# Kernel optimization log

Hardware: AMD Instinct MI355X
Metric: run time of the kernel (lower is better)

The kernel has to match this reference:

```python
import jax, jax.numpy as jnp
import numpy as np

NUM_GROUPS = 8
EPS = 1e-6


def group_norm(x, gamma, beta):
    # x: [B, C, N] flattened spatial; GroupNorm over (channels-in-group, spatial)
    B, C, N = x.shape
    xg = x.reshape(B, NUM_GROUPS, C // NUM_GROUPS, N)
    mean = xg.mean(axis=(2, 3), keepdims=True)
    var = xg.var(axis=(2, 3), keepdims=True)
    xn = ((xg - mean) * jax.lax.rsqrt(var + EPS)).reshape(B, C, N)
    return xn * gamma[None, :, None] + beta[None, :, None]


def setup_inputs() -> dict:
    key = jax.random.key(0)
    ks = jax.random.split(key, 3)
    B, C, H, W, D = 4, 128, 16, 16, 16
    x = jax.random.normal(ks[0], (B, C, H, W, D), dtype=jnp.float32)
    gamma = jnp.ones((C,), dtype=jnp.float32)
    beta = jnp.zeros((C,), dtype=jnp.float32)
    init_scale = 0.1
    # default_init(scale): variance-scaling ~ scale/fan_avg uniform; approximate with scaled normal
    w_qkv = jax.random.normal(ks[1], (3 * C, C), dtype=jnp.float32) * np.sqrt(init_scale / C)
    b_qkv = jnp.zeros((3 * C,), dtype=jnp.float32)
    w_proj = jax.random.normal(ks[2], (C, C), dtype=jnp.float32) * np.sqrt(init_scale / C)
    b_proj = jnp.zeros((C,), dtype=jnp.float32)
    return {"x": x, "gamma": gamma, "beta": beta, "w_qkv": w_qkv,
            "b_qkv": b_qkv, "w_proj": w_proj, "b_proj": b_proj}


def reference(x, gamma, beta, w_qkv, b_qkv, w_proj, b_proj):
    B, C, H, W, D = x.shape
    N = H * W * D
    xf = x.reshape(B, C, N)
    xn = group_norm(xf, gamma, beta)
    # 1x1 Conv3d == channel GEMM: [3C, C] @ [B, C, N]
    qkv = jnp.einsum('oc,bcn->bon', w_qkv, xn) + b_qkv[None, :, None]
    q, k, v = jnp.split(qkv, 3, axis=1)  # each [B, C, N]
    scale = float(C) ** (-0.5)
    w = jnp.einsum('bcq,bck->bqk', q, k) * scale  # [B, N, N]
    w = jax.nn.softmax(w, axis=-1)
    h = jnp.einsum('bqk,bck->bcq', w, v)  # [B, C, N]
    h = jnp.einsum('oc,bcn->bon', w_proj, h) + b_proj[None, :, None]
    out = xf + h  # skip_scale = 1.0 (skip_scale=False)
    return out.reshape(B, C, H, W, D)
```

## Files before the change

### kernel.cpp

```cpp
#include <hip/hip_runtime.h>

typedef __bf16 bf16_t;
typedef bf16_t bf16x8 __attribute__((ext_vector_type(8)));
typedef float f32x4 __attribute__((ext_vector_type(4)));
typedef unsigned short u16;
typedef unsigned int u32;

__device__ __forceinline__ float bfu2f(u32 h) {
  union { u32 u; float f; } v; v.u = h << 16;
  return v.f;
}
__device__ __forceinline__ void gll16(const void* g, void* l) {
  __builtin_amdgcn_global_load_lds((const __attribute__((address_space(1))) unsigned int*)g,
                                   (__attribute__((address_space(3))) unsigned int*)l, 16, 0, 0);
}

__global__ __launch_bounds__(256) void gn_stats(const float* __restrict__ x,
                                                float* __restrict__ partial) {
  int bg = blockIdx.x >> 4, ck = blockIdx.x & 15;
  int tid = threadIdx.x;
  const float4* base = reinterpret_cast<const float4*>(x + (size_t)bg * 65536 + ck * 4096);
  float s = 0.f, sq = 0.f;
  #pragma unroll
  for (int j = 0; j < 4; ++j) {
    float4 v = base[j * 256 + tid];
    s += v.x + v.y + v.z + v.w;
    sq += v.x * v.x + v.y * v.y + v.z * v.z + v.w * v.w;
  }
  #pragma unroll
  for (int off = 32; off > 0; off >>= 1) {
    s += __shfl_down(s, off);
    sq += __shfl_down(sq, off);
  }
  __shared__ float red[8];
  int wid = tid >> 6;
  if ((tid & 63) == 0) { red[wid] = s; red[4 + wid] = sq; }
  __syncthreads();
  if (tid == 0) {
    float ts = red[0] + red[1] + red[2] + red[3];
    float tq = red[4] + red[5] + red[6] + red[7];
    partial[(bg * 16 + ck) * 2] = ts;
    partial[(bg * 16 + ck) * 2 + 1] = tq;
  }
}

__global__ __launch_bounds__(256) void gn_norm(const float* __restrict__ x,
                                               const float* __restrict__ gamma,
                                               const float* __restrict__ beta,
                                               const float* __restrict__ partial,
                                               u16* __restrict__ xnt) {
  int bg = blockIdx.x >> 4, ck = blockIdx.x & 15;
  int b = bg >> 3, g = bg & 7;
  int tid = threadIdx.x;
  float s = 0.f, sq = 0.f;
  #pragma unroll
  for (int k = 0; k < 16; ++k) {
    s += partial[(bg * 16 + k) * 2];
    sq += partial[(bg * 16 + k) * 2 + 1];
  }
  float mean = s * (1.f / 65536.f);
  float var = sq * (1.f / 65536.f) - mean * mean;
  float rstd = rsqrtf(var + 1e-6f);
  int c_l = tid & 15;
  int c = g * 16 + c_l;
  float ga = gamma[c] * rstd;
  float be = beta[c] - mean * ga;
  const float* xr = x + ((size_t)(b * 128 + c)) * 4096;
  bf16_t* outb = (bf16_t*)(xnt + (size_t)b * 4096 * 128 + c);
  int n0 = ck * 256 + (tid >> 4);
  #pragma unroll
  for (int i = 0; i < 16; ++i) {
    int n = n0 + i * 16;
    outb[(size_t)n * 128] = (bf16_t)(xr[n] * ga + be);
  }
}

__global__ __launch_bounds__(256) void qkv_kernel(const float* __restrict__ wq,
                                                  const float* __restrict__ bq,
                                                  const u16* __restrict__ xnt,
                                                  u16* __restrict__ qt,
                                                  u16* __restrict__ kt,
                                                  u16* __restrict__ vv) {
  __shared__ char aS[16384];
  __shared__ char bS[16384];
  int b = blockIdx.z;
  int o0 = blockIdx.y * 64;
  int n0 = blockIdx.x * 64;
  int tid = threadIdx.x;
  #pragma unroll
  for (int i = 0; i < 8; ++i) {
    int chunk = tid + (i << 8);
    int o = chunk >> 5, cj = (chunk & 31) << 2;
    float4 f = *reinterpret_cast<const float4*>(wq + (o0 + o) * 128 + cj);
    u16 h0 = __builtin_bit_cast(u16, (bf16_t)f.x);
    u16 h1 = __builtin_bit_cast(u16, (bf16_t)f.y);
    u16 h2 = __builtin_bit_cast(u16, (bf16_t)f.z);
    u16 h3 = __builtin_bit_cast(u16, (bf16_t)f.w);
    ushort4 h4 = make_ushort4(h0, h1, h2, h3);
    *reinterpret_cast<ushort4*>(aS + ((o * 256 + cj * 2) ^ ((o & 7) << 4))) = h4;
  }
  #pragma unroll
  for (int i = 0; i < 4; ++i) {
    int chunk = tid + (i << 8);
    int n = chunk >> 4, ch = chunk & 15;
    uint4 d = *reinterpret_cast<const uint4*>(xnt + ((size_t)(b * 4096 + n0 + n)) * 128 + ch * 8);
    *reinterpret_cast<uint4*>(bS + ((n * 256 + ch * 16) ^ ((n & 7) << 4))) = d;
  }
  __syncthreads();
  int w = tid >> 6, l = tid & 63, lr = l & 15, lg = l >> 4;
  f32x4 acc[4] = {{0,0,0,0},{0,0,0,0},{0,0,0,0},{0,0,0,0}};
  int orow = 16 * w + lr;
  #pragma unroll
  for (int kc = 0; kc < 4; ++kc) {
    int c2 = (lg * 8 + 32 * kc) * 2;
    bf16x8 a = *reinterpret_cast<const bf16x8*>(aS + ((orow * 256 + c2) ^ ((orow & 7) << 4)));
    #pragma unroll
    for (int fn = 0; fn < 4; ++fn) {
      int n = lr + 16 * fn;
      bf16x8 bb = *reinterpret_cast<const bf16x8*>(bS + ((n * 256 + c2) ^ ((n & 7) << 4)));
      acc[fn] = __builtin_amdgcn_mfma_f32_16x16x32_bf16(a, bb, acc[fn], 0, 0, 0);
    }
  }
  const float alpha = 0.12753325f;
  #pragma unroll
  for (int fn = 0; fn < 4; ++fn) {
    #pragma unroll
    for (int j = 0; j < 4; ++j) {
      int o = o0 + 16 * w + lg * 4 + j;
      int n = n0 + lr + 16 * fn;
      float v = acc[fn][j] + bq[o];
      if (o < 128)      ((bf16_t*)qt)[((size_t)(b * 4096 + n)) * 128 + o] = (bf16_t)(v * alpha);
      else if (o < 256) ((bf16_t*)kt)[((size_t)(b * 4096 + n)) * 128 + (o - 128)] = (bf16_t)v;
      else              ((bf16_t*)vv)[((size_t)(b * 128 + (o - 256))) * 4096 + n] = (bf16_t)v;
    }
  }
}

__global__ __launch_bounds__(256) void attn_kernel(const u16* __restrict__ qt,
                                                   const u16* __restrict__ kt,
                                                   const u16* __restrict__ vv,
                                                   u16* __restrict__ opart,
                                                   float* __restrict__ ml) {
  __shared__ char kS[2][16384];
  __shared__ char vS[2][16384];
  __shared__ char pS[8192];
  int b = blockIdx.z;
  int sp = blockIdx.y;
  int q0 = blockIdx.x * 64;
  int tid = threadIdx.x;
  int w = tid >> 6, l = tid & 63, lr = l & 15, lg = l >> 4;

  bf16x8 qa[4];
  {
    const u16* qrow = qt + ((size_t)(b * 4096 + q0 + 16 * w + lr)) * 128 + lg * 8;
    #pragma unroll
    for (int kc = 0; kc < 4; ++kc)
      qa[kc] = *reinterpret_cast<const bf16x8*>(qrow + 32 * kc);
  }
  f32x4 acc[8];
  #pragma unroll
  for (int i = 0; i < 8; ++i) acc[i] = (f32x4){0.f, 0.f, 0.f, 0.f};
  float m2[4], lsum[4];
  #pragma unroll
  for (int j = 0; j < 4; ++j) { m2[j] = -1e30f; lsum[j] = 0.f; }

  const u16* ktb = kt + ((size_t)(b * 4096 + sp * 1024)) * 128;
  const u16* vvb = vv + ((size_t)b * 128) * 4096 + sp * 1024;

  auto stage = [&](int bufi, int kti) {
    #pragma unroll
    for (int i = 0; i < 4; ++i) {
      int n = (tid >> 4) + i * 16;
      int ck = (tid & 15) ^ (n & 7);
      gll16(ktb + (size_t)(kti * 64 + n) * 128 + ck * 8, kS[bufi] + tid * 16 + i * 4096);
    }
    #pragma unroll
    for (int i = 0; i < 4; ++i) {
      int c = (tid >> 3) + i * 32;
      int ck = (tid & 7) ^ (c & 7);
      gll16(vvb + (size_t)c * 4096 + kti * 64 + ck * 8, vS[bufi] + tid * 16 + i * 4096);
    }
  };

  stage(0, 0);
  __syncthreads();
  int buf = 0;

  for (int kti = 0; kti < 16; ++kti) {
    if (kti < 15) stage(buf ^ 1, kti + 1);

    f32x4 s[4];
    #pragma unroll
    for (int fn = 0; fn < 4; ++fn) s[fn] = (f32x4){0.f, 0.f, 0.f, 0.f};
    __builtin_amdgcn_s_setprio(1);
    #pragma unroll
    for (int kc = 0; kc < 4; ++kc) {
      int c2 = (lg * 8 + 32 * kc) * 2;
      bf16x8 a = qa[kc];
      #pragma unroll
      for (int fn = 0; fn < 4; ++fn) {
        int kp = lr + 16 * fn;
        bf16x8 bb = *reinterpret_cast<const bf16x8*>(kS[buf] + ((kp * 256 + c2) ^ ((kp & 7) << 4)));
        s[fn] = __builtin_amdgcn_mfma_f32_16x16x32_bf16(a, bb, s[fn], 0, 0, 0);
      }
    }
    __builtin_amdgcn_s_setprio(0);

    float mt[4];
    #pragma unroll
    for (int j = 0; j < 4; ++j)
      mt[j] = fmaxf(fmaxf(s[0][j], s[1][j]), fmaxf(s[2][j], s[3][j]));
    bool grow = (mt[0] > m2[0] + 8.f) || (mt[1] > m2[1] + 8.f) ||
                (mt[2] > m2[2] + 8.f) || (mt[3] > m2[3] + 8.f);
    if (__any(grow)) {
      #pragma unroll
      for (int off = 1; off < 16; off <<= 1)
        #pragma unroll
        for (int j = 0; j < 4; ++j)
          mt[j] = fmaxf(mt[j], __shfl_xor(mt[j], off));
      float r[4];
      #pragma unroll
      for (int j = 0; j < 4; ++j) {
        float mn = fmaxf(m2[j], mt[j]);
        r[j] = exp2f(m2[j] - mn);
        m2[j] = mn;
        lsum[j] *= r[j];
      }
      #pragma unroll
      for (int fc = 0; fc < 8; ++fc)
        #pragma unroll
        for (int j = 0; j < 4; ++j) acc[fc][j] *= r[j];
    }
    #pragma unroll
    for (int fn = 0; fn < 4; ++fn)
      #pragma unroll
      for (int j = 0; j < 4; ++j) {
        float p = exp2f(s[fn][j] - m2[j]);
        lsum[j] += p;
        int qg = 16 * w + lg * 4 + j;
        int kp = lr + 16 * fn;
        *reinterpret_cast<bf16_t*>(pS + ((qg * 128 + kp * 2) ^ ((qg & 7) << 4))) = (bf16_t)p;
      }
    __builtin_amdgcn_s_setprio(1);
    #pragma unroll
    for (int kc = 0; kc < 2; ++kc) {
      int qg = 16 * w + lr;
      int k2 = (lg * 8 + 32 * kc) * 2;
      bf16x8 pa = *reinterpret_cast<const bf16x8*>(pS + ((qg * 128 + k2) ^ ((qg & 7) << 4)));
      #pragma unroll
      for (int fc = 0; fc < 8; ++fc) {
        int c = lr + 16 * fc;
        bf16x8 vb = *reinterpret_cast<const bf16x8*>(vS[buf] + ((c * 128 + k2) ^ ((c & 7) << 4)));
        acc[fc] = __builtin_amdgcn_mfma_f32_16x16x32_bf16(pa, vb, acc[fc], 0, 0, 0);
      }
    }
    __builtin_amdgcn_s_setprio(0);
    __syncthreads();
    buf ^= 1;
  }
  #pragma unroll
  for (int off = 1; off < 16; off <<= 1)
    #pragma unroll
    for (int j = 0; j < 4; ++j)
      lsum[j] += __shfl_xor(lsum[j], off);
  #pragma unroll
  for (int j = 0; j < 4; ++j) {
    int nloc = 16 * w + lg * 4 + j;
    size_t row = (size_t)(sp * 16384 + b * 4096 + q0 + nloc);
    bf16_t* orow = (bf16_t*)(opart + row * 128 + lr);
    #pragma unroll
    for (int fc = 0; fc < 8; ++fc)
      orow[16 * fc] = (bf16_t)(acc[fc][j]);
    if (lr == 0) {
      ml[row * 2] = m2[j];
      ml[row * 2 + 1] = lsum[j];
    }
  }
}

__global__ __launch_bounds__(256) void proj_kernel(const float* __restrict__ wp,
                                                   const float* __restrict__ bp,
                                                   const u16* __restrict__ opart,
                                                   const float* __restrict__ ml,
                                                   const float* __restrict__ x,
                                                   float* __restrict__ out) {
  __shared__ char aS[16384];
  __shared__ char bS[16384];
  int b = blockIdx.z;
  int o0 = blockIdx.y * 64;
  int n0 = blockIdx.x * 64;
  int tid = threadIdx.x;
  #pragma unroll
  for (int i = 0; i < 8; ++i) {
    int chunk = tid + (i << 8);
    int o = chunk >> 5, cj = (chunk & 31) << 2;
    float4 f = *reinterpret_cast<const float4*>(wp + (o0 + o) * 128 + cj);
    u16 h0 = __builtin_bit_cast(u16, (bf16_t)f.x);
    u16 h1 = __builtin_bit_cast(u16, (bf16_t)f.y);
    u16 h2 = __builtin_bit_cast(u16, (bf16_t)f.z);
    u16 h3 = __builtin_bit_cast(u16, (bf16_t)f.w);
    *reinterpret_cast<ushort4*>(aS + ((o * 256 + cj * 2) ^ ((o & 7) << 4))) = make_ushort4(h0, h1, h2, h3);
  }
  #pragma unroll
  for (int i = 0; i < 4; ++i) {
    int chunk = tid + (i << 8);
    int n = chunk >> 4, ch = chunk & 15;
    size_t bn = (size_t)(b * 4096 + n0 + n);
    float m[4], lv[4];
    #pragma unroll
    for (int s = 0; s < 4; ++s) {
      m[s] = ml[((size_t)(s * 16384) + bn) * 2];
      lv[s] = ml[((size_t)(s * 16384) + bn) * 2 + 1];
    }
    float M = fmaxf(fmaxf(m[0], m[1]), fmaxf(m[2], m[3]));
    float wgt[4], L = 0.f;
    #pragma unroll
    for (int s = 0; s < 4; ++s) {
      wgt[s] = exp2f(m[s] - M);
      L += wgt[s] * lv[s];
    }
    float inv = 1.f / L;
    float o[8] = {0.f, 0.f, 0.f, 0.f, 0.f, 0.f, 0.f, 0.f};
    #pragma unroll
    for (int s = 0; s < 4; ++s) {
      uint4 pr = *reinterpret_cast<const uint4*>(opart + ((size_t)(s * 16384) + bn) * 128 + ch * 8);
      o[0] += wgt[s] * bfu2f(pr.x & 0xffffu);
      o[1] += wgt[s] * bfu2f(pr.x >> 16);
      o[2] += wgt[s] * bfu2f(pr.y & 0xffffu);
      o[3] += wgt[s] * bfu2f(pr.y >> 16);
      o[4] += wgt[s] * bfu2f(pr.z & 0xffffu);
      o[5] += wgt[s] * bfu2f(pr.z >> 16);
      o[6] += wgt[s] * bfu2f(pr.w & 0xffffu);
      o[7] += wgt[s] * bfu2f(pr.w >> 16);
    }
    u16 h[8];
    #pragma unroll
    for (int e = 0; e < 8; ++e) h[e] = __builtin_bit_cast(u16, (bf16_t)(o[e] * inv));
    uint4 packed;
    packed.x = (u32)h[0] | ((u32)h[1] << 16);
    packed.y = (u32)h[2] | ((u32)h[3] << 16);
    packed.z = (u32)h[4] | ((u32)h[5] << 16);
    packed.w = (u32)h[6] | ((u32)h[7] << 16);
    *reinterpret_cast<uint4*>(bS + ((n * 256 + ch * 16) ^ ((n & 7) << 4))) = packed;
  }
  __syncthreads();
  int w = tid >> 6, l = tid & 63, lr = l & 15, lg = l >> 4;
  f32x4 acc[4] = {{0,0,0,0},{0,0,0,0},{0,0,0,0},{0,0,0,0}};
  int orow = 16 * w + lr;
  #pragma unroll
  for (int kc = 0; kc < 4; ++kc) {
    int c2 = (lg * 8 + 32 * kc) * 2;
    bf16x8 a = *reinterpret_cast<const bf16x8*>(aS + ((orow * 256 + c2) ^ ((orow & 7) << 4)));
    #pragma unroll
    for (int fn = 0; fn < 4; ++fn) {
      int n = lr + 16 * fn;
      bf16x8 bb = *reinterpret_cast<const bf16x8*>(bS + ((n * 256 + c2) ^ ((n & 7) << 4)));
      acc[fn] = __builtin_amdgcn_mfma_f32_16x16x32_bf16(a, bb, acc[fn], 0, 0, 0);
    }
  }
  #pragma unroll
  for (int fn = 0; fn < 4; ++fn) {
    #pragma unroll
    for (int j = 0; j < 4; ++j) {
      int o = o0 + 16 * w + lg * 4 + j;
      int n = n0 + lr + 16 * fn;
      size_t idx = ((size_t)(b * 128 + o)) * 4096 + n;
      out[idx] = acc[fn][j] + bp[o] + x[idx];
    }
  }
}

extern "C" void kernel_launch(void* const* d_in, const int* in_sizes, int n_in,
                              void* d_out, int out_size, void* d_ws, size_t ws_size,
                              hipStream_t stream) {
  const float* x      = (const float*)d_in[0];
  const float* gamma  = (const float*)d_in[1];
  const float* beta   = (const float*)d_in[2];
  const float* w_qkv  = (const float*)d_in[3];
  const float* b_qkv  = (const float*)d_in[4];
  const float* w_proj = (const float*)d_in[5];
  const float* b_proj = (const float*)d_in[6];
  float* out = (float*)d_out;

  char* ws = (char*)d_ws;
  u16* xnt   = (u16*)(ws);
  u16* qt    = (u16*)(ws + (4u << 20));
  u16* kt    = (u16*)(ws + (8u << 20));
  u16* vv    = (u16*)(ws + (12u << 20));
  u16* opart = (u16*)(ws + (16u << 20));
  float* ml    = (float*)(ws + (48u << 20));
  float* parts = (float*)(ws + (49u << 20));

  hipLaunchKernelGGL(gn_stats, dim3(512), dim3(256), 0, stream, x, parts);
  hipLaunchKernelGGL(gn_norm, dim3(512), dim3(256), 0, stream, x, gamma, beta, parts, xnt);
  hipLaunchKernelGGL(qkv_kernel, dim3(64, 6, 4), dim3(256), 0, stream, w_qkv, b_qkv, xnt, qt, kt, vv);
  hipLaunchKernelGGL(attn_kernel, dim3(64, 4, 4), dim3(256), 0, stream, qt, kt, vv, opart, ml);
  hipLaunchKernelGGL(proj_kernel, dim3(64, 2, 4), dim3(256), 0, stream, w_proj, b_proj, opart, ml, x, out);
}
```

Measured before the change: 170.0 us.

## Switch attention to 32x32 MFMA with register-resident P and vectorize stores

The attention kernel now uses 32x32x16 bf16 MFMA with 128 query rows per block. It computes S transposed so the softmax probabilities can be repacked in registers through cross-lane shuffles, which removes the LDS round trip and the pS buffer. GroupNorm normalize and the Q/K epilogue of the QKV GEMM now write 16-byte vectorized transposed stores, the latter staged through shared memory. The attention grid is halved and launch bounds request two blocks per CU, which trades more registers per thread for fewer LDS accesses.

```diff
diff --git a/kernel.cpp b/kernel.cpp
--- a/kernel.cpp
+++ b/kernel.cpp
@@ -3,6 +3,7 @@
 typedef __bf16 bf16_t;
 typedef bf16_t bf16x8 __attribute__((ext_vector_type(8)));
 typedef float f32x4 __attribute__((ext_vector_type(4)));
+typedef float f32x16 __attribute__((ext_vector_type(16)));
 typedef unsigned short u16;
 typedef unsigned int u32;
 
@@ -13,6 +14,11 @@
 __device__ __forceinline__ void gll16(const void* g, void* l) {
   __builtin_amdgcn_global_load_lds((const __attribute__((address_space(1))) unsigned int*)g,
                                    (__attribute__((address_space(3))) unsigned int*)l, 16, 0, 0);
+}
+__device__ __forceinline__ u32 cvtpk(float lo, float hi) {
+  u32 r;
+  asm("v_cvt_pk_bf16_f32 %0, %1, %2" : "=v"(r) : "v"(lo), "v"(hi));
+  return r;
 }
 
 __global__ __launch_bounds__(256) void gn_stats(const float* __restrict__ x,
@@ -49,29 +55,36 @@
                                                const float* __restrict__ beta,
                                                const float* __restrict__ partial,
                                                u16* __restrict__ xnt) {
-  int bg = blockIdx.x >> 4, ck = blockIdx.x & 15;
-  int b = bg >> 3, g = bg & 7;
+  int b = blockIdx.x >> 6, nc = blockIdx.x & 63;
   int tid = threadIdx.x;
+  int cbase = (tid & 15) * 8;
+  int g = cbase >> 4;
   float s = 0.f, sq = 0.f;
   #pragma unroll
   for (int k = 0; k < 16; ++k) {
-    s += partial[(bg * 16 + k) * 2];
-    sq += partial[(bg * 16 + k) * 2 + 1];
+    s += partial[((b * 8 + g) * 16 + k) * 2];
+    sq += partial[((b * 8 + g) * 16 + k) * 2 + 1];
   }
   float mean = s * (1.f / 65536.f);
   float var = sq * (1.f / 65536.f) - mean * mean;
   float rstd = rsqrtf(var + 1e-6f);
-  int c_l = tid & 15;
-  int c = g * 16 + c_l;
-  float ga = gamma[c] * rstd;
-  float be = beta[c] - mean * ga;
-  const float* xr = x + ((size_t)(b * 128 + c)) * 4096;
-  bf16_t* outb = (bf16_t*)(xnt + (size_t)b * 4096 * 128 + c);
-  int n0 = ck * 256 + (tid >> 4);
-  #pragma unroll
-  for (int i = 0; i < 16; ++i) {
-    int n = n0 + i * 16;
-    outb[(size_t)n * 128] = (bf16_t)(xr[n] * ga + be);
+  float ga[8], be[8];
+  #pragma unroll
+  for (int j = 0; j < 8; ++j) {
+    ga[j] = gamma[cbase + j] * rstd;
+    be[j] = beta[cbase + j] - mean * ga[j];
+  }
+  int n0 = nc * 64;
+  #pragma unroll
+  for (int it = 0; it < 4; ++it) {
+    int n = n0 + it * 16 + (tid >> 4);
+    union { u16 s[8]; uint4 u; } pk;
+    #pragma unroll
+    for (int j = 0; j < 8; ++j) {
+      float v = x[((size_t)(b * 128 + cbase + j)) * 4096 + n] * ga[j] + be[j];
+      pk.s[j] = __builtin_bit_cast(u16, (bf16_t)v);
+    }
+    *reinterpret_cast<uint4*>(xnt + ((size_t)(b * 4096 + n)) * 128 + cbase) = pk.u;
   }
 }
 
@@ -96,8 +109,7 @@
     u16 h1 = __builtin_bit_cast(u16, (bf16_t)f.y);
     u16 h2 = __builtin_bit_cast(u16, (bf16_t)f.z);
     u16 h3 = __builtin_bit_cast(u16, (bf16_t)f.w);
-    ushort4 h4 = make_ushort4(h0, h1, h2, h3);
-    *reinterpret_cast<ushort4*>(aS + ((o * 256 + cj * 2) ^ ((o & 7) << 4))) = h4;
+    *reinterpret_cast<ushort4*>(aS + ((o * 256 + cj * 2) ^ ((o & 7) << 4))) = make_ushort4(h0, h1, h2, h3);
   }
   #pragma unroll
   for (int i = 0; i < 4; ++i) {
@@ -122,47 +134,73 @@
     }
   }
   const float alpha = 0.12753325f;
-  #pragma unroll
-  for (int fn = 0; fn < 4; ++fn) {
-    #pragma unroll
-    for (int j = 0; j < 4; ++j) {
-      int o = o0 + 16 * w + lg * 4 + j;
-      int n = n0 + lr + 16 * fn;
-      float v = acc[fn][j] + bq[o];
-      if (o < 128)      ((bf16_t*)qt)[((size_t)(b * 4096 + n)) * 128 + o] = (bf16_t)(v * alpha);
-      else if (o < 256) ((bf16_t*)kt)[((size_t)(b * 4096 + n)) * 128 + (o - 128)] = (bf16_t)v;
-      else              ((bf16_t*)vv)[((size_t)(b * 128 + (o - 256))) * 4096 + n] = (bf16_t)v;
-    }
-  }
-}
-
-__global__ __launch_bounds__(256) void attn_kernel(const u16* __restrict__ qt,
-                                                   const u16* __restrict__ kt,
-                                                   const u16* __restrict__ vv,
-                                                   u16* __restrict__ opart,
-                                                   float* __restrict__ ml) {
+  if (o0 < 256) {
+    bool isq = (o0 < 128);
+    __syncthreads();
+    u16* tS = (u16*)aS;
+    #pragma unroll
+    for (int fn = 0; fn < 4; ++fn) {
+      #pragma unroll
+      for (int j = 0; j < 4; ++j) {
+        int o_loc = 16 * w + lg * 4 + j;
+        int n_loc = lr + 16 * fn;
+        float v = acc[fn][j] + bq[o0 + o_loc];
+        if (isq) v *= alpha;
+        tS[o_loc * 68 + n_loc] = __builtin_bit_cast(u16, (bf16_t)v);
+      }
+    }
+    __syncthreads();
+    u16* dst = isq ? qt : kt;
+    int obase = o0 & 127;
+    #pragma unroll
+    for (int it = 0; it < 2; ++it) {
+      int n_l = (tid >> 3) + it * 32;
+      int oc = (tid & 7) * 8;
+      union { u16 s[8]; uint4 u; } pk;
+      #pragma unroll
+      for (int k2 = 0; k2 < 8; ++k2) pk.s[k2] = tS[(oc + k2) * 68 + n_l];
+      *reinterpret_cast<uint4*>(dst + ((size_t)(b * 4096 + n0 + n_l)) * 128 + obase + oc) = pk.u;
+    }
+  } else {
+    #pragma unroll
+    for (int fn = 0; fn < 4; ++fn) {
+      #pragma unroll
+      for (int j = 0; j < 4; ++j) {
+        int o_loc = 16 * w + lg * 4 + j;
+        int n = n0 + lr + 16 * fn;
+        float v = acc[fn][j] + bq[o0 + o_loc];
+        ((bf16_t*)vv)[((size_t)(b * 128 + (o0 - 256) + o_loc)) * 4096 + n] = (bf16_t)v;
+      }
+    }
+  }
+}
+
+__global__ __launch_bounds__(256, 2) void attn_kernel(const u16* __restrict__ qt,
+                                                      const u16* __restrict__ kt,
+                                                      const u16* __restrict__ vv,
+                                                      u16* __restrict__ opart,
+                                                      float* __restrict__ ml) {
   __shared__ char kS[2][16384];
   __shared__ char vS[2][16384];
-  __shared__ char pS[8192];
   int b = blockIdx.z;
   int sp = blockIdx.y;
-  int q0 = blockIdx.x * 64;
+  int q0 = blockIdx.x * 128;
   int tid = threadIdx.x;
-  int w = tid >> 6, l = tid & 63, lr = l & 15, lg = l >> 4;
-
-  bf16x8 qa[4];
+  int w = tid >> 6, l = tid & 63, lq = l & 31, h = l >> 5;
+
+  bf16x8 qf[8];
   {
-    const u16* qrow = qt + ((size_t)(b * 4096 + q0 + 16 * w + lr)) * 128 + lg * 8;
-    #pragma unroll
-    for (int kc = 0; kc < 4; ++kc)
-      qa[kc] = *reinterpret_cast<const bf16x8*>(qrow + 32 * kc);
-  }
-  f32x4 acc[8];
-  #pragma unroll
-  for (int i = 0; i < 8; ++i) acc[i] = (f32x4){0.f, 0.f, 0.f, 0.f};
-  float m2[4], lsum[4];
-  #pragma unroll
-  for (int j = 0; j < 4; ++j) { m2[j] = -1e30f; lsum[j] = 0.f; }
+    const u16* qrow = qt + ((size_t)(b * 4096 + q0 + w * 32 + lq)) * 128 + h * 8;
+    #pragma unroll
+    for (int cs = 0; cs < 8; ++cs)
+      qf[cs] = *reinterpret_cast<const bf16x8*>(qrow + cs * 16);
+  }
+  f32x16 acc[4];
+  #pragma unroll
+  for (int cc = 0; cc < 4; ++cc)
+    #pragma unroll
+    for (int i = 0; i < 16; ++i) acc[cc][i] = 0.f;
+  float m2 = -1e30f, lsum = 0.f;
 
   const u16* ktb = kt + ((size_t)(b * 4096 + sp * 1024)) * 128;
   const u16* vvb = vv + ((size_t)b * 128) * 4096 + sp * 1024;
@@ -189,92 +227,98 @@
   for (int kti = 0; kti < 16; ++kti) {
     if (kti < 15) stage(buf ^ 1, kti + 1);
 
-    f32x4 s[4];
-    #pragma unroll
-    for (int fn = 0; fn < 4; ++fn) s[fn] = (f32x4){0.f, 0.f, 0.f, 0.f};
+    f32x16 st0, st1;
+    #pragma unroll
+    for (int i = 0; i < 16; ++i) { st0[i] = 0.f; st1[i] = 0.f; }
     __builtin_amdgcn_s_setprio(1);
     #pragma unroll
-    for (int kc = 0; kc < 4; ++kc) {
-      int c2 = (lg * 8 + 32 * kc) * 2;
-      bf16x8 a = qa[kc];
-      #pragma unroll
-      for (int fn = 0; fn < 4; ++fn) {
-        int kp = lr + 16 * fn;
-        bf16x8 bb = *reinterpret_cast<const bf16x8*>(kS[buf] + ((kp * 256 + c2) ^ ((kp & 7) << 4)));
-        s[fn] = __builtin_amdgcn_mfma_f32_16x16x32_bf16(a, bb, s[fn], 0, 0, 0);
-      }
+    for (int cs = 0; cs < 8; ++cs) {
+      int co = cs * 32 + h * 16;
+      bf16x8 kf0 = *reinterpret_cast<const bf16x8*>(kS[buf] + ((lq * 256 + co) ^ ((lq & 7) << 4)));
+      st0 = __builtin_amdgcn_mfma_f32_32x32x16_bf16(kf0, qf[cs], st0, 0, 0, 0);
+      int kr1 = 32 + lq;
+      bf16x8 kf1 = *reinterpret_cast<const bf16x8*>(kS[buf] + ((kr1 * 256 + co) ^ ((kr1 & 7) << 4)));
+      st1 = __builtin_amdgcn_mfma_f32_32x32x16_bf16(kf1, qf[cs], st1, 0, 0, 0);
     }
     __builtin_amdgcn_s_setprio(0);
 
-    float mt[4];
-    #pragma unroll
-    for (int j = 0; j < 4; ++j)
-      mt[j] = fmaxf(fmaxf(s[0][j], s[1][j]), fmaxf(s[2][j], s[3][j]));
-    bool grow = (mt[0] > m2[0] + 8.f) || (mt[1] > m2[1] + 8.f) ||
-                (mt[2] > m2[2] + 8.f) || (mt[3] > m2[3] + 8.f);
-    if (__any(grow)) {
-      #pragma unroll
-      for (int off = 1; off < 16; off <<= 1)
+    float mt = st0[0];
+    #pragma unroll
+    for (int i = 1; i < 16; ++i) mt = fmaxf(mt, st0[i]);
+    #pragma unroll
+    for (int i = 0; i < 16; ++i) mt = fmaxf(mt, st1[i]);
+    mt = fmaxf(mt, __shfl_xor(mt, 32));
+    if (__any(mt > m2 + 8.f)) {
+      float mn = fmaxf(m2, mt);
+      float r = exp2f(m2 - mn);
+      m2 = mn;
+      lsum *= r;
+      #pragma unroll
+      for (int reg = 0; reg < 16; ++reg) {
+        int qrow = (reg & 3) + 8 * (reg >> 2) + 4 * h;
+        float rq = __shfl(r, qrow);
         #pragma unroll
-        for (int j = 0; j < 4; ++j)
-          mt[j] = fmaxf(mt[j], __shfl_xor(mt[j], off));
-      float r[4];
-      #pragma unroll
-      for (int j = 0; j < 4; ++j) {
-        float mn = fmaxf(m2[j], mt[j]);
-        r[j] = exp2f(m2[j] - mn);
-        m2[j] = mn;
-        lsum[j] *= r[j];
-      }
-      #pragma unroll
-      for (int fc = 0; fc < 8; ++fc)
-        #pragma unroll
-        for (int j = 0; j < 4; ++j) acc[fc][j] *= r[j];
-    }
-    #pragma unroll
-    for (int fn = 0; fn < 4; ++fn)
-      #pragma unroll
-      for (int j = 0; j < 4; ++j) {
-        float p = exp2f(s[fn][j] - m2[j]);
-        lsum[j] += p;
-        int qg = 16 * w + lg * 4 + j;
-        int kp = lr + 16 * fn;
-        *reinterpret_cast<bf16_t*>(pS + ((qg * 128 + kp * 2) ^ ((qg & 7) << 4))) = (bf16_t)p;
-      }
+        for (int cc = 0; cc < 4; ++cc) acc[cc][reg] *= rq;
+      }
+    }
+    bf16x8 pa[4];
+    #pragma unroll
+    for (int ks = 0; ks < 2; ++ks) {
+      float p[16];
+      #pragma unroll
+      for (int i = 0; i < 16; ++i) {
+        float sv = (ks == 0) ? st0[i] : st1[i];
+        p[i] = exp2f(sv - m2);
+        lsum += p[i];
+      }
+      #pragma unroll
+      for (int kk = 0; kk < 2; ++kk) {
+        int r0 = kk * 8, r1 = kk * 8 + 4;
+        u32 a1 = cvtpk(p[r0 + 0], p[r0 + 1]);
+        u32 a2 = cvtpk(p[r0 + 2], p[r0 + 3]);
+        u32 b1 = cvtpk(p[r1 + 0], p[r1 + 1]);
+        u32 b2 = cvtpk(p[r1 + 2], p[r1 + 3]);
+        u32 sa1 = (u32)__shfl_xor((int)a1, 32);
+        u32 sa2 = (u32)__shfl_xor((int)a2, 32);
+        u32 sb1 = (u32)__shfl_xor((int)b1, 32);
+        u32 sb2 = (u32)__shfl_xor((int)b2, 32);
+        union { u32 wd[4]; bf16x8 v; } af;
+        af.wd[0] = h ? sb1 : a1;
+        af.wd[1] = h ? sb2 : a2;
+        af.wd[2] = h ? b1 : sa1;
+        af.wd[3] = h ? b2 : sa2;
+        pa[ks * 2 + kk] = af.v;
+      }
+    }
     __builtin_amdgcn_s_setprio(1);
     #pragma unroll
-    for (int kc = 0; kc < 2; ++kc) {
-      int qg = 16 * w + lr;
-      int k2 = (lg * 8 + 32 * kc) * 2;
-      bf16x8 pa = *reinterpret_cast<const bf16x8*>(pS + ((qg * 128 + k2) ^ ((qg & 7) << 4)));
-      #pragma unroll
-      for (int fc = 0; fc < 8; ++fc) {
-        int c = lr + 16 * fc;
-        bf16x8 vb = *reinterpret_cast<const bf16x8*>(vS[buf] + ((c * 128 + k2) ^ ((c & 7) << 4)));
-        acc[fc] = __builtin_amdgcn_mfma_f32_16x16x32_bf16(pa, vb, acc[fc], 0, 0, 0);
+    for (int ks2 = 0; ks2 < 4; ++ks2) {
+      int ko = ks2 * 32 + h * 16;
+      #pragma unroll
+      for (int cc = 0; cc < 4; ++cc) {
+        int c = cc * 32 + lq;
+        bf16x8 vf = *reinterpret_cast<const bf16x8*>(vS[buf] + ((c * 128 + ko) ^ ((c & 7) << 4)));
+        acc[cc] = __builtin_amdgcn_mfma_f32_32x32x16_bf16(pa[ks2], vf, acc[cc], 0, 0, 0);
       }
     }
     __builtin_amdgcn_s_setprio(0);
     __syncthreads();
     buf ^= 1;
   }
-  #pragma unroll
-  for (int off = 1; off < 16; off <<= 1)
-    #pragma unroll
-    for (int j = 0; j < 4; ++j)
-      lsum[j] += __shfl_xor(lsum[j], off);
-  #pragma unroll
-  for (int j = 0; j < 4; ++j) {
-    int nloc = 16 * w + lg * 4 + j;
-    size_t row = (size_t)(sp * 16384 + b * 4096 + q0 + nloc);
-    bf16_t* orow = (bf16_t*)(opart + row * 128 + lr);
-    #pragma unroll
-    for (int fc = 0; fc < 8; ++fc)
-      orow[16 * fc] = (bf16_t)(acc[fc][j]);
-    if (lr == 0) {
-      ml[row * 2] = m2[j];
-      ml[row * 2 + 1] = lsum[j];
-    }
+  lsum += __shfl_xor(lsum, 32);
+  #pragma unroll
+  for (int reg = 0; reg < 16; ++reg) {
+    int qrow = (reg & 3) + 8 * (reg >> 2) + 4 * h;
+    size_t row = (size_t)(sp * 16384 + b * 4096 + q0 + w * 32 + qrow);
+    bf16_t* orow = (bf16_t*)opart + row * 128 + lq;
+    #pragma unroll
+    for (int cc = 0; cc < 4; ++cc)
+      orow[cc * 32] = (bf16_t)acc[cc][reg];
+  }
+  if (l < 32) {
+    size_t row = (size_t)(sp * 16384 + b * 4096 + q0 + w * 32 + l);
+    ml[row * 2] = m2;
+    ml[row * 2 + 1] = lsum;
   }
 }
 
@@ -333,14 +377,14 @@
       o[6] += wgt[s] * bfu2f(pr.w & 0xffffu);
       o[7] += wgt[s] * bfu2f(pr.w >> 16);
     }
-    u16 h[8];
-    #pragma unroll
-    for (int e = 0; e < 8; ++e) h[e] = __builtin_bit_cast(u16, (bf16_t)(o[e] * inv));
+    u16 hh[8];
+    #pragma unroll
+    for (int e = 0; e < 8; ++e) hh[e] = __builtin_bit_cast(u16, (bf16_t)(o[e] * inv));
     uint4 packed;
-    packed.x = (u32)h[0] | ((u32)h[1] << 16);
-    packed.y = (u32)h[2] | ((u32)h[3] << 16);
-    packed.z = (u32)h[4] | ((u32)h[5] << 16);
-    packed.w = (u32)h[6] | ((u32)h[7] << 16);
+    packed.x = (u32)hh[0] | ((u32)hh[1] << 16);
+    packed.y = (u32)hh[2] | ((u32)hh[3] << 16);
+    packed.z = (u32)hh[4] | ((u32)hh[5] << 16);
+    packed.w = (u32)hh[6] | ((u32)hh[7] << 16);
     *reinterpret_cast<uint4*>(bS + ((n * 256 + ch * 16) ^ ((n & 7) << 4))) = packed;
   }
   __syncthreads();
@@ -392,8 +436,8 @@
   float* parts = (float*)(ws + (49u << 20));
 
   hipLaunchKernelGGL(gn_stats, dim3(512), dim3(256), 0, stream, x, parts);
-  hipLaunchKernelGGL(gn_norm, dim3(512), dim3(256), 0, stream, x, gamma, beta, parts, xnt);
+  hipLaunchKernelGGL(gn_norm, dim3(256), dim3(256), 0, stream, x, gamma, beta, parts, xnt);
   hipLaunchKernelGGL(qkv_kernel, dim3(64, 6, 4), dim3(256), 0, stream, w_qkv, b_qkv, xnt, qt, kt, vv);
-  hipLaunchKernelGGL(attn_kernel, dim3(64, 4, 4), dim3(256), 0, stream, qt, kt, vv, opart, ml);
+  hipLaunchKernelGGL(attn_kernel, dim3(32, 4, 4), dim3(256), 0, stream, qt, kt, vv, opart, ml);
   hipLaunchKernelGGL(proj_kernel, dim3(64, 2, 4), dim3(256), 0, stream, w_proj, b_proj, opart, ml, x, out);
 }
```

Result: faster. 142.4 us (-16.3%).
